# Kernel tuning notes

Hardware: AMD Instinct MI355X
Metric: run time of the kernel (lower is better)

The kernel has to match this reference:

```python
import jax, jax.numpy as jnp
import numpy as np


def _seg_mean(feat, dst, n):
    # mean aggregation of gathered source features onto destination nodes
    s = jax.ops.segment_sum(feat, dst, num_segments=n)
    c = jax.ops.segment_sum(jnp.ones((dst.shape[0], 1), feat.dtype), dst, num_segments=n)
    return s / jnp.maximum(c, 1.0)


def setup_inputs() -> dict:
    key = jax.random.key(0)
    ks = jax.random.split(key, 16)
    N0, N1, N2 = 400000, 100000, 25000
    E0, E1 = 1600000, 400000
    IN, HID, OUT = 128, 256, 64
    inp = {
        "x_tar": jax.random.normal(ks[0], (N0, IN), jnp.float32),
        "x_neigh": jax.random.normal(ks[1], (N0, IN), jnp.float32),
        "edge_src0": jax.random.randint(ks[2], (E0,), 0, N0, jnp.int64).astype(jnp.int32),
        "edge_dst0": jax.random.randint(ks[3], (E0,), 0, N1, jnp.int64).astype(jnp.int32),
        "edge_src1": jax.random.randint(ks[4], (E1,), 0, N1, jnp.int64).astype(jnp.int32),
        "edge_dst1": jax.random.randint(ks[5], (E1,), 0, N2, jnp.int64).astype(jnp.int32),
        "n_dst0": N1,
        "n_dst1": N2,
    }
    s = 1.0 / np.sqrt(IN)
    sh = 1.0 / np.sqrt(HID)
    inp["Wl0"] = jax.random.uniform(ks[6], (IN, HID), jnp.float32, -s, s)
    inp["Wr0"] = jax.random.uniform(ks[7], (IN, HID), jnp.float32, -s, s)
    inp["b0"] = jnp.zeros((HID,), jnp.float32)
    inp["Wl1"] = jax.random.uniform(ks[8], (HID, HID), jnp.float32, -sh, sh)
    inp["Wr1"] = jax.random.uniform(ks[9], (HID, HID), jnp.float32, -sh, sh)
    inp["b1"] = jnp.zeros((HID,), jnp.float32)
    inp["Wl2"] = jax.random.uniform(ks[10], (HID, OUT), jnp.float32, -sh, sh)
    inp["Wr2"] = jax.random.uniform(ks[11], (HID, OUT), jnp.float32, -sh, sh)
    inp["b2"] = jnp.zeros((OUT,), jnp.float32)
    return inp


def reference(x_tar, x_neigh, edge_src0, edge_dst0, edge_src1, edge_dst1,
              n_dst0, n_dst1, Wl0, Wr0, b0, Wl1, Wr1, b1, Wl2, Wr2, b2):
    # layer 0: precomputed neighbor aggregation -> lin_l(x_neigh) + lin_r(x_tar)
    x = x_neigh @ Wl0 + x_tar @ Wr0 + b0  # [N0, HID]
    # layer 1: bipartite mean-aggregate SAGEConv + relu (eval mode: dropout is identity)
    x_t = x[:n_dst0]
    aggr = _seg_mean(x[edge_src0], edge_dst0, n_dst0)
    x = jax.nn.relu(aggr @ Wl1 + x_t @ Wr1 + b1)  # [N1, HID]
    # layer 2: final SAGEConv
    x_t = x[:n_dst1]
    aggr = _seg_mean(x[edge_src1], edge_dst1, n_dst1)
    out = aggr @ Wl2 + x_t @ Wr2 + b2  # [N2, OUT]
    return jax.nn.log_softmax(out, axis=-1)
```

## Files before the change

kernel.cpp:

```cpp
#include <hip/hip_runtime.h>
#include <hip/hip_bf16.h>

typedef __bf16 bf16_t;
typedef __bf16 bf16x8_t __attribute__((ext_vector_type(8)));
typedef __bf16 bf16x4_t __attribute__((ext_vector_type(4)));
typedef float  f32x4_t  __attribute__((ext_vector_type(4)));

#define N1_ROWS 100000
#define N2_ROWS 25000
#define DIN  128
#define DHID 256
#define DOUT 64
#define CAP  96

__global__ __launch_bounds__(256) void transpose_w(
    const float* __restrict__ W, bf16_t* __restrict__ WT, int K, int N) {
  int gid = blockIdx.x * 256 + threadIdx.x;
  if (gid >= K * N) return;
  int n = gid / K, k = gid - n * K;
  WT[gid] = (bf16_t)W[k * N + n];
}

template<int BN, bool RELU, bool OUTF32, bool AF32>
__global__ __launch_bounds__(256) void gemm_dual(
    const void* __restrict__ A1v, const void* __restrict__ A2v,
    const bf16_t* __restrict__ W1T, const bf16_t* __restrict__ W2T,
    const float* __restrict__ bias, void* __restrict__ outp,
    int M, int K1, int K2) {
  constexpr int BM = 64, BK = 32;
  __shared__ bf16_t sA[BM * BK];
  __shared__ bf16_t sB[BN * BK];
  const int tid  = threadIdx.x;
  const int wave = tid >> 6, lane = tid & 63;
  const int l15  = lane & 15, quad = lane >> 4;
  const int rowBase = blockIdx.x * BM;

  f32x4_t acc[BN / 16];
#pragma unroll
  for (int t = 0; t < BN / 16; ++t) acc[t] = (f32x4_t){0.f, 0.f, 0.f, 0.f};

  const int ldr = tid >> 2;
  const int ldk = (tid & 3) * 8;

  for (int half = 0; half < 2; ++half) {
    const void* A  = half ? A2v : A1v;
    const bf16_t* WT = half ? W2T : W1T;
    const int K = half ? K2 : K1;
    for (int k0 = 0; k0 < K; k0 += BK) {
      __syncthreads();
      {
        int gr = rowBase + ldr; if (gr >= M) gr = M - 1;
        if (AF32) {
          const float* Af = (const float*)A;
          float4 lo = *(const float4*)&Af[(size_t)gr * K + k0 + ldk];
          float4 hi = *(const float4*)&Af[(size_t)gr * K + k0 + ldk + 4];
          bf16x8_t v;
          v[0] = (bf16_t)lo.x; v[1] = (bf16_t)lo.y; v[2] = (bf16_t)lo.z; v[3] = (bf16_t)lo.w;
          v[4] = (bf16_t)hi.x; v[5] = (bf16_t)hi.y; v[6] = (bf16_t)hi.z; v[7] = (bf16_t)hi.w;
          *(bf16x8_t*)&sA[ldr * BK + ldk] = v;
        } else {
          const bf16_t* Ab = (const bf16_t*)A;
          *(uint4*)&sA[ldr * BK + ldk] = *(const uint4*)&Ab[(size_t)gr * K + k0 + ldk];
        }
      }
#pragma unroll
      for (int p = 0; p < BN / 64; ++p) {
        int r = p * 64 + ldr;
        *(uint4*)&sB[r * BK + ldk] = *(const uint4*)&WT[(size_t)r * K + k0 + ldk];
      }
      __syncthreads();
      bf16x8_t a = *(const bf16x8_t*)&sA[(wave * 16 + l15) * BK + quad * 8];
#pragma unroll
      for (int t = 0; t < BN / 16; ++t) {
        bf16x8_t b = *(const bf16x8_t*)&sB[(t * 16 + l15) * BK + quad * 8];
        acc[t] = __builtin_amdgcn_mfma_f32_16x16x32_bf16(a, b, acc[t], 0, 0, 0);
      }
    }
  }

  const int rbase = rowBase + wave * 16 + quad * 4;
#pragma unroll
  for (int t = 0; t < BN / 16; ++t) {
    int col = t * 16 + l15;
    float bv = bias[col];
#pragma unroll
    for (int i = 0; i < 4; ++i) {
      int row = rbase + i;
      if (row < M) {
        float v = acc[t][i] + bv;
        if (RELU) v = fmaxf(v, 0.f);
        if (OUTF32) ((float*)outp)[(size_t)row * BN + col] = v;
        else        ((bf16_t*)outp)[(size_t)row * BN + col] = (bf16_t)v;
      }
    }
  }
}

__global__ __launch_bounds__(256) void csr_append(
    const int* __restrict__ src, const int* __restrict__ dst,
    int* __restrict__ cnt, int* __restrict__ csr, int E) {
  int e = blockIdx.x * 256 + threadIdx.x;
  if (e >= E) return;
  int d = dst[e];
  int pos = atomicAdd(&cnt[d], 1);
  if (pos < CAP) csr[(size_t)d * CAP + pos] = src[e];
}

__global__ __launch_bounds__(256) void gather_mean(
    const bf16_t* __restrict__ X, const int* __restrict__ csr,
    const int* __restrict__ cnt, bf16_t* __restrict__ outp, int n) {
  int gid = blockIdx.x * 256 + threadIdx.x;
  int d = gid >> 6, lane = gid & 63;
  if (d >= n) return;
  int deg = cnt[d]; if (deg > CAP) deg = CAP;
  const int* bucket = csr + (size_t)d * CAP;
  float a0 = 0.f, a1 = 0.f, a2 = 0.f, a3 = 0.f;
  for (int i = 0; i < deg; ++i) {
    int s = bucket[i];
    bf16x4_t v = *(const bf16x4_t*)(X + (size_t)s * DHID + lane * 4);
    a0 += (float)v[0]; a1 += (float)v[1]; a2 += (float)v[2]; a3 += (float)v[3];
  }
  float inv = 1.f / (float)(deg > 0 ? deg : 1);
  bf16x4_t o;
  o[0] = (bf16_t)(a0 * inv); o[1] = (bf16_t)(a1 * inv);
  o[2] = (bf16_t)(a2 * inv); o[3] = (bf16_t)(a3 * inv);
  *(bf16x4_t*)(outp + (size_t)d * DHID + lane * 4) = o;
}

__global__ __launch_bounds__(256) void log_softmax64(
    float* __restrict__ logits, int R) {
  int gid = blockIdx.x * 256 + threadIdx.x;
  int row = gid >> 6, lane = gid & 63;
  if (row >= R) return;
  float v = logits[(size_t)row * DOUT + lane];
  float m = v;
  for (int o = 32; o > 0; o >>= 1) m = fmaxf(m, __shfl_xor(m, o, 64));
  float e = expf(v - m);
  float s = e;
  for (int o = 32; o > 0; o >>= 1) s += __shfl_xor(s, o, 64);
  logits[(size_t)row * DOUT + lane] = v - m - logf(s);
}

extern "C" void kernel_launch(void* const* d_in, const int* in_sizes, int n_in,
                              void* d_out, int out_size, void* d_ws, size_t ws_size,
                              hipStream_t stream) {
  const float* x_tar   = (const float*)d_in[0];
  const float* x_neigh = (const float*)d_in[1];
  const int* es0 = (const int*)d_in[2];
  const int* ed0 = (const int*)d_in[3];
  const int* es1 = (const int*)d_in[4];
  const int* ed1 = (const int*)d_in[5];
  const float* Wl0 = (const float*)d_in[8];
  const float* Wr0 = (const float*)d_in[9];
  const float* b0  = (const float*)d_in[10];
  const float* Wl1 = (const float*)d_in[11];
  const float* Wr1 = (const float*)d_in[12];
  const float* b1  = (const float*)d_in[13];
  const float* Wl2 = (const float*)d_in[14];
  const float* Wr2 = (const float*)d_in[15];
  const float* b2  = (const float*)d_in[16];

  const int E0 = in_sizes[2];
  const int E1 = in_sizes[4];
  const int M0 = in_sizes[0] / DIN;

  char* ws = (char*)d_ws;
  bf16_t* Wl0T = (bf16_t*)(ws + 0);
  bf16_t* Wr0T = (bf16_t*)(ws + 65536);
  bf16_t* Wl1T = (bf16_t*)(ws + 131072);
  bf16_t* Wr1T = (bf16_t*)(ws + 262144);
  bf16_t* Wl2T = (bf16_t*)(ws + 393216);
  bf16_t* Wr2T = (bf16_t*)(ws + 425984);
  bf16_t* x0     = (bf16_t*)(ws + 524288);
  bf16_t* x1     = (bf16_t*)(ws + 524288 + 51200000);
  bf16_t* aggrB  = (bf16_t*)(ws + 205324288);
  bf16_t* aggr2B = (bf16_t*)(ws + 256524288);
  int*    csr0   = (int*)(ws + 269324288);
  int*    csr1   = (int*)(ws + 307724288);
  int*    cnt0   = (int*)(ws + 317324288);
  int*    cnt1   = (int*)(ws + 317724288);
  float*  logits = (float*)d_out;

  transpose_w<<<(DIN * DHID + 255) / 256, 256, 0, stream>>>(Wl0, Wl0T, DIN, DHID);
  transpose_w<<<(DIN * DHID + 255) / 256, 256, 0, stream>>>(Wr0, Wr0T, DIN, DHID);
  transpose_w<<<(DHID * DHID + 255) / 256, 256, 0, stream>>>(Wl1, Wl1T, DHID, DHID);
  transpose_w<<<(DHID * DHID + 255) / 256, 256, 0, stream>>>(Wr1, Wr1T, DHID, DHID);
  transpose_w<<<(DHID * DOUT + 255) / 256, 256, 0, stream>>>(Wl2, Wl2T, DHID, DOUT);
  transpose_w<<<(DHID * DOUT + 255) / 256, 256, 0, stream>>>(Wr2, Wr2T, DHID, DOUT);

  hipMemsetAsync(cnt0, 0, (size_t)N1_ROWS * 4, stream);
  hipMemsetAsync(cnt1, 0, (size_t)N2_ROWS * 4, stream);

  csr_append<<<(E0 + 255) / 256, 256, 0, stream>>>(es0, ed0, cnt0, csr0, E0);

  gemm_dual<DHID, false, false, true><<<(M0 + 63) / 64, 256, 0, stream>>>(
      x_neigh, x_tar, Wl0T, Wr0T, b0, x0, M0, DIN, DIN);

  gather_mean<<<(int)(((long long)N1_ROWS * 64 + 255) / 256), 256, 0, stream>>>(
      x0, csr0, cnt0, aggrB, N1_ROWS);

  gemm_dual<DHID, true, false, false><<<(N1_ROWS + 63) / 64, 256, 0, stream>>>(
      aggrB, x0, Wl1T, Wr1T, b1, x1, N1_ROWS, DHID, DHID);

  csr_append<<<(E1 + 255) / 256, 256, 0, stream>>>(es1, ed1, cnt1, csr1, E1);

  gather_mean<<<(int)(((long long)N2_ROWS * 64 + 255) / 256), 256, 0, stream>>>(
      x1, csr1, cnt1, aggr2B, N2_ROWS);

  gemm_dual<DOUT, false, true, false><<<(N2_ROWS + 63) / 64, 256, 0, stream>>>(
      aggr2B, x1, Wl2T, Wr2T, b2, logits, N2_ROWS, DHID, DHID);

  log_softmax64<<<(int)(((long long)N2_ROWS * 64 + 255) / 256), 256, 0, stream>>>(
      logits, N2_ROWS);
}
```

Before: 1.101 ms.

## Restructure GEMM tiling, batch prep and CSR kernels, unroll gather loop

The GEMM now has each wave own a column slice, loading its B fragments straight from global memory into registers, while all four waves share a padded LDS tile of A and compute a 4xNT block of MFMA tiles. This removes the B staging through LDS and raises MFMA work per LDS load. The six weight-transpose launches become one kernel, the two CSR builds become one launch with a single memset, and the gather loop is unrolled by four with separate accumulators so more loads are in flight. The risks are higher register pressure and uncoalesced global B loads per wave.

```diff
diff --git a/kernel.cpp b/kernel.cpp
--- a/kernel.cpp
+++ b/kernel.cpp
@@ -13,97 +13,126 @@
 #define DOUT 64
 #define CAP  96
 
-__global__ __launch_bounds__(256) void transpose_w(
-    const float* __restrict__ W, bf16_t* __restrict__ WT, int K, int N) {
-  int gid = blockIdx.x * 256 + threadIdx.x;
-  if (gid >= K * N) return;
+__global__ __launch_bounds__(256) void prep_weights(
+    const float* __restrict__ Wl0, const float* __restrict__ Wr0,
+    const float* __restrict__ Wl1, const float* __restrict__ Wr1,
+    const float* __restrict__ Wl2, const float* __restrict__ Wr2,
+    bf16_t* __restrict__ Wl0T, bf16_t* __restrict__ Wr0T,
+    bf16_t* __restrict__ Wl1T, bf16_t* __restrict__ Wr1T,
+    bf16_t* __restrict__ Wl2T, bf16_t* __restrict__ Wr2T) {
+  int b = blockIdx.x;
+  const float* W; bf16_t* WT; int K, N, base;
+  if      (b < 128) { W = Wl0; WT = Wl0T; K = 128; N = 256; base = 0;   }
+  else if (b < 256) { W = Wr0; WT = Wr0T; K = 128; N = 256; base = 128; }
+  else if (b < 512) { W = Wl1; WT = Wl1T; K = 256; N = 256; base = 256; }
+  else if (b < 768) { W = Wr1; WT = Wr1T; K = 256; N = 256; base = 512; }
+  else if (b < 832) { W = Wl2; WT = Wl2T; K = 256; N = 64;  base = 768; }
+  else              { W = Wr2; WT = Wr2T; K = 256; N = 64;  base = 832; }
+  int gid = (b - base) * 256 + threadIdx.x;
   int n = gid / K, k = gid - n * K;
-  WT[gid] = (bf16_t)W[k * N + n];
-}
-
-template<int BN, bool RELU, bool OUTF32, bool AF32>
-__global__ __launch_bounds__(256) void gemm_dual(
+  WT[gid] = (bf16_t)W[(size_t)k * N + n];
+}
+
+template<int NT, bool RELU, bool OUTF32, bool AF32>
+__global__ __launch_bounds__(256) void gemm_fast(
     const void* __restrict__ A1v, const void* __restrict__ A2v,
     const bf16_t* __restrict__ W1T, const bf16_t* __restrict__ W2T,
     const float* __restrict__ bias, void* __restrict__ outp,
     int M, int K1, int K2) {
-  constexpr int BM = 64, BK = 32;
-  __shared__ bf16_t sA[BM * BK];
-  __shared__ bf16_t sB[BN * BK];
+  constexpr int BK = 32;
+  constexpr int LDA = 40;
+  __shared__ bf16_t sA[64 * LDA];
   const int tid  = threadIdx.x;
   const int wave = tid >> 6, lane = tid & 63;
   const int l15  = lane & 15, quad = lane >> 4;
-  const int rowBase = blockIdx.x * BM;
-
-  f32x4_t acc[BN / 16];
-#pragma unroll
-  for (int t = 0; t < BN / 16; ++t) acc[t] = (f32x4_t){0.f, 0.f, 0.f, 0.f};
-
-  const int ldr = tid >> 2;
-  const int ldk = (tid & 3) * 8;
+  const int rowBase = blockIdx.x * 64;
+  const int colBase = wave * (NT * 16);
+  constexpr int NOUT = NT * 64;
+
+  f32x4_t acc[4][NT];
+#pragma unroll
+  for (int mt = 0; mt < 4; ++mt)
+#pragma unroll
+    for (int nt = 0; nt < NT; ++nt) acc[mt][nt] = (f32x4_t){0.f, 0.f, 0.f, 0.f};
+
+  const int sr = tid >> 2;
+  const int sc = (tid & 3) * 8;
+  int gr = rowBase + sr; if (gr >= M) gr = M - 1;
 
   for (int half = 0; half < 2; ++half) {
-    const void* A  = half ? A2v : A1v;
+    const void* A = half ? A2v : A1v;
     const bf16_t* WT = half ? W2T : W1T;
     const int K = half ? K2 : K1;
     for (int k0 = 0; k0 < K; k0 += BK) {
+      bf16x8_t bf[NT];
+#pragma unroll
+      for (int nt = 0; nt < NT; ++nt)
+        bf[nt] = *(const bf16x8_t*)&WT[(size_t)(colBase + nt * 16 + l15) * K + k0 + quad * 8];
       __syncthreads();
-      {
-        int gr = rowBase + ldr; if (gr >= M) gr = M - 1;
-        if (AF32) {
-          const float* Af = (const float*)A;
-          float4 lo = *(const float4*)&Af[(size_t)gr * K + k0 + ldk];
-          float4 hi = *(const float4*)&Af[(size_t)gr * K + k0 + ldk + 4];
-          bf16x8_t v;
-          v[0] = (bf16_t)lo.x; v[1] = (bf16_t)lo.y; v[2] = (bf16_t)lo.z; v[3] = (bf16_t)lo.w;
-          v[4] = (bf16_t)hi.x; v[5] = (bf16_t)hi.y; v[6] = (bf16_t)hi.z; v[7] = (bf16_t)hi.w;
-          *(bf16x8_t*)&sA[ldr * BK + ldk] = v;
-        } else {
-          const bf16_t* Ab = (const bf16_t*)A;
-          *(uint4*)&sA[ldr * BK + ldk] = *(const uint4*)&Ab[(size_t)gr * K + k0 + ldk];
+      if (AF32) {
+        const float* Af = (const float*)A;
+        float4 lo = *(const float4*)&Af[(size_t)gr * K + k0 + sc];
+        float4 hi = *(const float4*)&Af[(size_t)gr * K + k0 + sc + 4];
+        bf16x8_t v;
+        v[0] = (bf16_t)lo.x; v[1] = (bf16_t)lo.y; v[2] = (bf16_t)lo.z; v[3] = (bf16_t)lo.w;
+        v[4] = (bf16_t)hi.x; v[5] = (bf16_t)hi.y; v[6] = (bf16_t)hi.z; v[7] = (bf16_t)hi.w;
+        *(bf16x8_t*)&sA[sr * LDA + sc] = v;
+      } else {
+        *(uint4*)&sA[sr * LDA + sc] =
+            *(const uint4*)&((const bf16_t*)A)[(size_t)gr * K + k0 + sc];
+      }
+      __syncthreads();
+#pragma unroll
+      for (int mt = 0; mt < 4; ++mt) {
+        bf16x8_t af = *(const bf16x8_t*)&sA[(mt * 16 + l15) * LDA + quad * 8];
+#pragma unroll
+        for (int nt = 0; nt < NT; ++nt)
+          acc[mt][nt] = __builtin_amdgcn_mfma_f32_16x16x32_bf16(af, bf[nt], acc[mt][nt], 0, 0, 0);
+      }
+    }
+  }
+
+  const int rb = rowBase + quad * 4;
+#pragma unroll
+  for (int mt = 0; mt < 4; ++mt)
+#pragma unroll
+    for (int nt = 0; nt < NT; ++nt) {
+      int col = colBase + nt * 16 + l15;
+      float bv = bias[col];
+#pragma unroll
+      for (int i = 0; i < 4; ++i) {
+        int row = rb + mt * 16 + i;
+        if (row < M) {
+          float v = acc[mt][nt][i] + bv;
+          if (RELU) v = fmaxf(v, 0.f);
+          if (OUTF32) ((float*)outp)[(size_t)row * NOUT + col] = v;
+          else        ((bf16_t*)outp)[(size_t)row * NOUT + col] = (bf16_t)v;
         }
       }
-#pragma unroll
-      for (int p = 0; p < BN / 64; ++p) {
-        int r = p * 64 + ldr;
-        *(uint4*)&sB[r * BK + ldk] = *(const uint4*)&WT[(size_t)r * K + k0 + ldk];
-      }
-      __syncthreads();
-      bf16x8_t a = *(const bf16x8_t*)&sA[(wave * 16 + l15) * BK + quad * 8];
-#pragma unroll
-      for (int t = 0; t < BN / 16; ++t) {
-        bf16x8_t b = *(const bf16x8_t*)&sB[(t * 16 + l15) * BK + quad * 8];
-        acc[t] = __builtin_amdgcn_mfma_f32_16x16x32_bf16(a, b, acc[t], 0, 0, 0);
-      }
-    }
-  }
-
-  const int rbase = rowBase + wave * 16 + quad * 4;
-#pragma unroll
-  for (int t = 0; t < BN / 16; ++t) {
-    int col = t * 16 + l15;
-    float bv = bias[col];
-#pragma unroll
-    for (int i = 0; i < 4; ++i) {
-      int row = rbase + i;
-      if (row < M) {
-        float v = acc[t][i] + bv;
-        if (RELU) v = fmaxf(v, 0.f);
-        if (OUTF32) ((float*)outp)[(size_t)row * BN + col] = v;
-        else        ((bf16_t*)outp)[(size_t)row * BN + col] = (bf16_t)v;
-      }
-    }
-  }
-}
-
-__global__ __launch_bounds__(256) void csr_append(
-    const int* __restrict__ src, const int* __restrict__ dst,
-    int* __restrict__ cnt, int* __restrict__ csr, int E) {
-  int e = blockIdx.x * 256 + threadIdx.x;
-  if (e >= E) return;
-  int d = dst[e];
-  int pos = atomicAdd(&cnt[d], 1);
-  if (pos < CAP) csr[(size_t)d * CAP + pos] = src[e];
+    }
+}
+
+__global__ __launch_bounds__(256) void csr_append2(
+    const int* __restrict__ s0, const int* __restrict__ d0, int E0,
+    int* __restrict__ cnt0, int* __restrict__ csr0,
+    const int* __restrict__ s1, const int* __restrict__ d1, int E1,
+    int* __restrict__ cnt1, int* __restrict__ csr1, int B0) {
+  int b = blockIdx.x;
+  if (b < B0) {
+    int e = b * 256 + threadIdx.x;
+    if (e < E0) {
+      int d = d0[e];
+      int pos = atomicAdd(&cnt0[d], 1);
+      if (pos < CAP) csr0[(size_t)d * CAP + pos] = s0[e];
+    }
+  } else {
+    int e = (b - B0) * 256 + threadIdx.x;
+    if (e < E1) {
+      int d = d1[e];
+      int pos = atomicAdd(&cnt1[d], 1);
+      if (pos < CAP) csr1[(size_t)d * CAP + pos] = s1[e];
+    }
+  }
 }
 
 __global__ __launch_bounds__(256) void gather_mean(
@@ -114,16 +143,31 @@
   if (d >= n) return;
   int deg = cnt[d]; if (deg > CAP) deg = CAP;
   const int* bucket = csr + (size_t)d * CAP;
-  float a0 = 0.f, a1 = 0.f, a2 = 0.f, a3 = 0.f;
-  for (int i = 0; i < deg; ++i) {
+  f32x4_t A0 = {0,0,0,0}, A1 = {0,0,0,0}, A2 = {0,0,0,0}, A3 = {0,0,0,0};
+  int i = 0;
+  for (; i + 4 <= deg; i += 4) {
+    int s0 = bucket[i], s1 = bucket[i+1], s2 = bucket[i+2], s3 = bucket[i+3];
+    bf16x4_t v0 = *(const bf16x4_t*)(X + (size_t)s0 * DHID + lane * 4);
+    bf16x4_t v1 = *(const bf16x4_t*)(X + (size_t)s1 * DHID + lane * 4);
+    bf16x4_t v2 = *(const bf16x4_t*)(X + (size_t)s2 * DHID + lane * 4);
+    bf16x4_t v3 = *(const bf16x4_t*)(X + (size_t)s3 * DHID + lane * 4);
+#pragma unroll
+    for (int j = 0; j < 4; ++j) {
+      A0[j] += (float)v0[j]; A1[j] += (float)v1[j];
+      A2[j] += (float)v2[j]; A3[j] += (float)v3[j];
+    }
+  }
+  for (; i < deg; ++i) {
     int s = bucket[i];
     bf16x4_t v = *(const bf16x4_t*)(X + (size_t)s * DHID + lane * 4);
-    a0 += (float)v[0]; a1 += (float)v[1]; a2 += (float)v[2]; a3 += (float)v[3];
+#pragma unroll
+    for (int j = 0; j < 4; ++j) A0[j] += (float)v[j];
   }
   float inv = 1.f / (float)(deg > 0 ? deg : 1);
   bf16x4_t o;
-  o[0] = (bf16_t)(a0 * inv); o[1] = (bf16_t)(a1 * inv);
-  o[2] = (bf16_t)(a2 * inv); o[3] = (bf16_t)(a3 * inv);
+#pragma unroll
+  for (int j = 0; j < 4; ++j)
+    o[j] = (bf16_t)((A0[j] + A1[j] + A2[j] + A3[j]) * inv);
   *(bf16x4_t*)(outp + (size_t)d * DHID + lane * 4) = o;
 }
 
@@ -181,33 +225,30 @@
   int*    cnt1   = (int*)(ws + 317724288);
   float*  logits = (float*)d_out;
 
-  transpose_w<<<(DIN * DHID + 255) / 256, 256, 0, stream>>>(Wl0, Wl0T, DIN, DHID);
-  transpose_w<<<(DIN * DHID + 255) / 256, 256, 0, stream>>>(Wr0, Wr0T, DIN, DHID);
-  transpose_w<<<(DHID * DHID + 255) / 256, 256, 0, stream>>>(Wl1, Wl1T, DHID, DHID);
-  transpose_w<<<(DHID * DHID + 255) / 256, 256, 0, stream>>>(Wr1, Wr1T, DHID, DHID);
-  transpose_w<<<(DHID * DOUT + 255) / 256, 256, 0, stream>>>(Wl2, Wl2T, DHID, DOUT);
-  transpose_w<<<(DHID * DOUT + 255) / 256, 256, 0, stream>>>(Wr2, Wr2T, DHID, DOUT);
-
-  hipMemsetAsync(cnt0, 0, (size_t)N1_ROWS * 4, stream);
-  hipMemsetAsync(cnt1, 0, (size_t)N2_ROWS * 4, stream);
-
-  csr_append<<<(E0 + 255) / 256, 256, 0, stream>>>(es0, ed0, cnt0, csr0, E0);
-
-  gemm_dual<DHID, false, false, true><<<(M0 + 63) / 64, 256, 0, stream>>>(
+  prep_weights<<<896, 256, 0, stream>>>(Wl0, Wr0, Wl1, Wr1, Wl2, Wr2,
+                                        Wl0T, Wr0T, Wl1T, Wr1T, Wl2T, Wr2T);
+
+  hipMemsetAsync(cnt0, 0, (size_t)(N1_ROWS + N2_ROWS) * 4, stream);
+
+  {
+    int B0 = (E0 + 255) / 256, B1 = (E1 + 255) / 256;
+    csr_append2<<<B0 + B1, 256, 0, stream>>>(es0, ed0, E0, cnt0, csr0,
+                                             es1, ed1, E1, cnt1, csr1, B0);
+  }
+
+  gemm_fast<4, false, false, true><<<(M0 + 63) / 64, 256, 0, stream>>>(
       x_neigh, x_tar, Wl0T, Wr0T, b0, x0, M0, DIN, DIN);
 
   gather_mean<<<(int)(((long long)N1_ROWS * 64 + 255) / 256), 256, 0, stream>>>(
       x0, csr0, cnt0, aggrB, N1_ROWS);
 
-  gemm_dual<DHID, true, false, false><<<(N1_ROWS + 63) / 64, 256, 0, stream>>>(
+  gemm_fast<4, true, false, false><<<(N1_ROWS + 63) / 64, 256, 0, stream>>>(
       aggrB, x0, Wl1T, Wr1T, b1, x1, N1_ROWS, DHID, DHID);
-
-  csr_append<<<(E1 + 255) / 256, 256, 0, stream>>>(es1, ed1, cnt1, csr1, E1);
 
   gather_mean<<<(int)(((long long)N2_ROWS * 64 + 255) / 256), 256, 0, stream>>>(
       x1, csr1, cnt1, aggr2B, N2_ROWS);
 
-  gemm_dual<DOUT, false, true, false><<<(N2_ROWS + 63) / 64, 256, 0, stream>>>(
+  gemm_fast<1, false, true, false><<<(N2_ROWS + 63) / 64, 256, 0, stream>>>(
       aggr2B, x1, Wl2T, Wr2T, b2, logits, N2_ROWS, DHID, DHID);
 
   log_softmax64<<<(int)(((long long)N2_ROWS * 64 + 255) / 256), 256, 0, stream>>>(
```

Measured after the change: 953.2 us. 1.16x faster.
